# Kernel tuning notes

Measured on AMD Instinct MI355X. Metric: run time of the kernel, lower is better.

Reference implementation:

```python
import jax, jax.numpy as jnp
import numpy as np

KEY_DIM = 64
SCALE_PER_SEQ = 1.0 / np.sqrt(KEY_DIM).astype(np.float32)   # attn_scale_factor_per_seq default
SCALE_OVER_SEQS = 1.0 / np.sqrt(KEY_DIM).astype(np.float32) # attn_scale_factor_over_seqs default


def setup_inputs() -> dict:
    key = jax.random.key(0)
    ks = jax.random.split(key, 6)
    b, i, t, j, d = 8, 256, 64, 256, 256
    kd, vd = KEY_DIM, 64
    return {
        "input_seq": jax.random.normal(ks[0], (b, i, d), dtype=jnp.float32),
        "memory_x": jax.random.normal(ks[1], (b, t, j, d), dtype=jnp.float32),
        "memory_y": jax.random.normal(ks[2], (b, t, j, d), dtype=jnp.float32),
        "Wq": jax.random.normal(ks[3], (d, kd), dtype=jnp.float32) * (1.0 / np.sqrt(d)),
        "bq": jnp.zeros((kd,), dtype=jnp.float32),
        "Wk": jax.random.normal(ks[4], (d, kd), dtype=jnp.float32) * (1.0 / np.sqrt(d)),
        "bk": jnp.zeros((kd,), dtype=jnp.float32),
        "Wv": jax.random.normal(ks[5], (d, vd), dtype=jnp.float32) * (1.0 / np.sqrt(d)),
        "bv": jnp.zeros((vd,), dtype=jnp.float32),
    }


def reference(input_seq, memory_x, memory_y, Wq, bq, Wk, bk, Wv, bv):
    # Dense projections
    queries = input_seq @ Wq + bq            # [b, i, kd]
    keys = memory_x @ Wk + bk                # [b, t, j, kd]
    values = memory_y @ Wv + bv              # [b, t, j, vd]

    # Raw scores between every query and every token of every memory sequence
    attn_mat = jnp.einsum('bik,btjk->btij', queries, keys)  # [b, t, i, j]

    # Level 1: within-sequence attention (softmax over tokens j)
    per_seq_attn = jax.nn.softmax(SCALE_PER_SEQ * attn_mat, axis=-1)
    per_seq_retrieved = jnp.einsum('btij,btjk->btik', per_seq_attn, values)  # [b, t, i, vd]

    # Level 2: over-sequences attention (max over j, softmax over t)
    mem_seq_scores = jnp.max(attn_mat, axis=-1)                      # [b, t, i]
    mem_seq_attn = jax.nn.softmax(SCALE_OVER_SEQS * mem_seq_scores, axis=1)

    retrieved_mems = jnp.einsum('bti,btik->bik', mem_seq_attn, per_seq_retrieved)  # [b, i, vd]
    return retrieved_mems
```

## Files before the change

### kernel.cpp

```cpp
#include <hip/hip_runtime.h>
#include <hip/hip_bf16.h>

#define NB 8
#define NT 64
#define NI 256
#define NJ 256
#define ND 256
#define NKD 64
#define NVD 64
#define SCL 0.125f

typedef __attribute__((ext_vector_type(4))) float f32x4;
typedef __attribute__((ext_vector_type(8))) short bf16x8;
typedef __attribute__((ext_vector_type(4))) short bf16x4;
typedef __attribute__((ext_vector_type(4))) unsigned int uint32x4;

#define MFMA16(A, B, C) __builtin_amdgcn_mfma_f32_16x16x32_bf16((A), (B), (C), 0, 0, 0)

#define R2B 32768

__device__ __forceinline__ unsigned short f2bf(float x) {
  return __builtin_bit_cast(unsigned short, __float2bfloat16(x));
}
__device__ __forceinline__ float bf2f(unsigned short h) {
  return __builtin_bit_cast(float, (unsigned)h << 16);
}
__device__ __forceinline__ void split8(const float* __restrict__ x, bf16x8& hi, bf16x8& lo) {
  #pragma unroll
  for (int e = 0; e < 8; ++e) {
    unsigned short h = f2bf(x[e]);
    hi[e] = (short)h;
    lo[e] = (short)f2bf(x[e] - bf2f(h));
  }
}

__global__ __launch_bounds__(64) void k_prep_projq(
    const float* __restrict__ x, const float* __restrict__ Wq,
    const float* __restrict__ bq,
    const float* __restrict__ Wk, const float* __restrict__ Wv,
    unsigned short* __restrict__ Wkth,
    unsigned short* __restrict__ Wvth, unsigned short* __restrict__ Wvtl,
    unsigned short* __restrict__ Qh, unsigned short* __restrict__ Ql) {
  int lane = threadIdx.x;
  if (blockIdx.x < 256) {
    int t = blockIdx.x * 64 + lane;
    int d = t >> 6, kd = t & 63;
    Wkth[kd * 256 + d] = f2bf(Wk[t]);
    float v = Wv[t];
    unsigned short h = f2bf(v);
    Wvth[kd * 256 + d] = h;
    Wvtl[kd * 256 + d] = f2bf(v - bf2f(h));
    return;
  }
  int row = blockIdx.x - 256;
  __shared__ __align__(16) float xs[ND];
  const float* xr = x + (size_t)row * ND;
  #pragma unroll
  for (int cc = 0; cc < 4; ++cc) xs[lane + 64 * cc] = xr[lane + 64 * cc];
  __syncthreads();
  float acc = bq[lane];
  #pragma unroll 4
  for (int d = 0; d < ND; ++d) acc = fmaf(xs[d], Wq[d * NKD + lane], acc);
  unsigned short h = f2bf(acc);
  Qh[(size_t)row * NKD + lane] = h;
  Ql[(size_t)row * NKD + lane] = f2bf(acc - bf2f(h));
}

__device__ __forceinline__ void stage_plane(
    char* dstb, const unsigned short* __restrict__ Wt, int tid) {
  #pragma unroll
  for (int it = 0; it < 4; ++it) {
    int qq = tid + it * 512;
    int r = qq >> 5, pb = qq & 31;
    uint4 v = *(const uint4*)((const char*)Wt + (size_t)qq * 16);
    *(uint4*)(dstb + r * 512 + ((pb ^ (r & 7)) << 4)) = v;
  }
}

__global__ __launch_bounds__(512, 4) void k_fused(
    const float* __restrict__ Xm, const float* __restrict__ Ym,
    const unsigned short* __restrict__ Wkth,
    const unsigned short* __restrict__ Wvth, const unsigned short* __restrict__ Wvtl,
    const float* __restrict__ bk, const float* __restrict__ bv,
    const unsigned short* __restrict__ Qh, const unsigned short* __restrict__ Ql,
    unsigned short* __restrict__ R,
    float* __restrict__ Sc) {
  __shared__ __align__(16) char smemb[65536];
  int tid = threadIdx.x;
  int bt = blockIdx.x, b = bt >> 6;
  int w = tid >> 6, lane = tid & 63, c = lane & 15, g = lane >> 4;

  const float* yr0 = Ym + (size_t)bt * 65536 + (size_t)(w * 32 + c) * 256 + g * 8;
  const float* yr1 = yr0 + 16 * 256;
  const float* xr0 = Xm + (size_t)bt * 65536 + (size_t)(w * 32 + c) * 256 + g * 8;
  const float* xr1 = xr0 + 16 * 256;

  float4 pby[4][4];
  #pragma unroll
  for (int s = 0; s < 4; ++s) {
    pby[s][0] = *(const float4*)(yr0 + s * 32);
    pby[s][1] = *(const float4*)(yr0 + s * 32 + 4);
    pby[s][2] = *(const float4*)(yr1 + s * 32);
    pby[s][3] = *(const float4*)(yr1 + s * 32 + 4);
  }
  stage_plane(smemb, Wvth, tid);
  stage_plane(smemb + R2B, Wvtl, tid);
  __syncthreads();

  f32x4 vacc[2][4];
  #pragma unroll
  for (int mf = 0; mf < 2; ++mf)
    #pragma unroll
    for (int nf = 0; nf < 4; ++nf) vacc[mf][nf] = (f32x4)0.f;
  #pragma unroll
  for (int ks = 0; ks < 8; ++ks) {
    int s = ks & 3;
    float y0[8], y1[8];
    *(float4*)&y0[0] = pby[s][0]; *(float4*)&y0[4] = pby[s][1];
    *(float4*)&y1[0] = pby[s][2]; *(float4*)&y1[4] = pby[s][3];
    if (ks < 4) {
      pby[s][0] = *(const float4*)(yr0 + (ks + 4) * 32);
      pby[s][1] = *(const float4*)(yr0 + (ks + 4) * 32 + 4);
      pby[s][2] = *(const float4*)(yr1 + (ks + 4) * 32);
      pby[s][3] = *(const float4*)(yr1 + (ks + 4) * 32 + 4);
    }
    bf16x8 a0h, a0l, a1h, a1l;
    split8(y0, a0h, a0l);
    split8(y1, a1h, a1l);
    #pragma unroll
    for (int nf = 0; nf < 4; ++nf) {
      int r = nf * 16 + c;
      int ba = r * 512 + (((ks * 4 + g) ^ (r & 7)) << 4);
      bf16x8 bwh = *(const bf16x8*)(smemb + ba);
      bf16x8 bwl = *(const bf16x8*)(smemb + R2B + ba);
      vacc[0][nf] = MFMA16(a0h, bwh, vacc[0][nf]);
      vacc[0][nf] = MFMA16(a0l, bwh, vacc[0][nf]);
      vacc[0][nf] = MFMA16(a0h, bwl, vacc[0][nf]);
      vacc[1][nf] = MFMA16(a1h, bwh, vacc[1][nf]);
      vacc[1][nf] = MFMA16(a1l, bwh, vacc[1][nf]);
      vacc[1][nf] = MFMA16(a1h, bwl, vacc[1][nf]);
    }
  }
  __syncthreads();

  float4 pbx[4][4];
  #pragma unroll
  for (int s = 0; s < 4; ++s) {
    pbx[s][0] = *(const float4*)(xr0 + s * 32);
    pbx[s][1] = *(const float4*)(xr0 + s * 32 + 4);
    pbx[s][2] = *(const float4*)(xr1 + s * 32);
    pbx[s][3] = *(const float4*)(xr1 + s * 32 + 4);
  }
  #pragma unroll
  for (int nf = 0; nf < 4; ++nf) {
    int vd = nf * 16 + c;
    float bs = bv[vd];
    #pragma unroll
    for (int mf = 0; mf < 2; ++mf) {
      bf16x4 ph;
      #pragma unroll
      for (int r = 0; r < 4; ++r) ph[r] = (short)f2bf(vacc[mf][nf][r] + bs);
      int pb = w * 4 + mf * 2 + (g >> 1);
      int ba = R2B + vd * 512 + ((pb ^ (vd & 7)) << 4) + (g & 1) * 8;
      *(bf16x4*)(smemb + ba) = ph;
    }
  }
  stage_plane(smemb, Wkth, tid);
  __syncthreads();

  f32x4 kacc[4][2];
  #pragma unroll
  for (int mf = 0; mf < 4; ++mf) { kacc[mf][0] = (f32x4)0.f; kacc[mf][1] = (f32x4)0.f; }
  #pragma unroll
  for (int ks = 0; ks < 8; ++ks) {
    int s = ks & 3;
    float x0[8], x1[8];
    *(float4*)&x0[0] = pbx[s][0]; *(float4*)&x0[4] = pbx[s][1];
    *(float4*)&x1[0] = pbx[s][2]; *(float4*)&x1[4] = pbx[s][3];
    if (ks < 4) {
      pbx[s][0] = *(const float4*)(xr0 + (ks + 4) * 32);
      pbx[s][1] = *(const float4*)(xr0 + (ks + 4) * 32 + 4);
      pbx[s][2] = *(const float4*)(xr1 + (ks + 4) * 32);
      pbx[s][3] = *(const float4*)(xr1 + (ks + 4) * 32 + 4);
    }
    bf16x8 b0h, b0l, b1h, b1l;
    split8(x0, b0h, b0l);
    split8(x1, b1h, b1l);
    #pragma unroll
    for (int mf = 0; mf < 4; ++mf) {
      int r = mf * 16 + c;
      int ba = r * 512 + (((ks * 4 + g) ^ (r & 7)) << 4);
      bf16x8 awh = *(const bf16x8*)(smemb + ba);
      kacc[mf][0] = MFMA16(awh, b0h, kacc[mf][0]);
      kacc[mf][0] = MFMA16(awh, b0l, kacc[mf][0]);
      kacc[mf][1] = MFMA16(awh, b1h, kacc[mf][1]);
      kacc[mf][1] = MFMA16(awh, b1l, kacc[mf][1]);
    }
  }
  __syncthreads();

  bf16x8 qbh[2][2], qbl[2][2];
  #pragma unroll
  for (int ks = 0; ks < 2; ++ks)
    #pragma unroll
    for (int ic = 0; ic < 2; ++ic) {
      size_t qo = ((size_t)b * NI + w * 32 + ic * 16 + c) * NKD + ks * 32 + g * 8;
      qbh[ks][ic] = *(const bf16x8*)(Qh + qo);
      qbl[ks][ic] = *(const bf16x8*)(Ql + qo);
    }
  #pragma unroll
  for (int nf = 0; nf < 2; ++nf) {
    int j = w * 32 + nf * 16 + c;
    #pragma unroll
    for (int mf = 0; mf < 4; ++mf) {
      bf16x4 ph;
      #pragma unroll
      for (int r = 0; r < 4; ++r)
        ph[r] = (short)f2bf(kacc[mf][nf][r] + bk[mf * 16 + g * 4 + r]);
      int pb = mf * 2 + (g >> 1);
      int ba = j * 128 + ((pb ^ (j & 7)) << 4) + (g & 1) * 8;
      *(bf16x4*)(smemb + ba) = ph;
    }
  }
  __syncthreads();

  #pragma unroll
  for (int ic = 0; ic < 2; ++ic) {
    int i = w * 32 + ic * 16 + c;

    f32x4 sa[16];
    #pragma unroll
    for (int jf = 0; jf < 16; ++jf) sa[jf] = (f32x4)0.f;
    #pragma unroll
    for (int jf = 0; jf < 16; ++jf) {
      int j = jf * 16 + c;
      #pragma unroll
      for (int ks = 0; ks < 2; ++ks) {
        int ba = j * 128 + (((ks * 4 + g) ^ (j & 7)) << 4);
        bf16x8 kh = *(const bf16x8*)(smemb + ba);
        sa[jf] = MFMA16(kh, qbh[ks][ic], sa[jf]);
        sa[jf] = MFMA16(kh, qbl[ks][ic], sa[jf]);
      }
    }

    float mx = sa[0][0];
    #pragma unroll
    for (int jf = 0; jf < 16; ++jf)
      #pragma unroll
      for (int r = 0; r < 4; ++r) mx = fmaxf(mx, sa[jf][r]);
    mx = fmaxf(mx, __shfl_xor(mx, 16));
    mx = fmaxf(mx, __shfl_xor(mx, 32));
    if (g == 0) Sc[(size_t)bt * NI + i] = mx;
    float sum = 0.f;
    #pragma unroll
    for (int jf = 0; jf < 16; ++jf)
      #pragma unroll
      for (int r = 0; r < 4; ++r) {
        float p = __expf((sa[jf][r] - mx) * SCL);
        sa[jf][r] = p;
        sum += p;
      }
    sum += __shfl_xor(sum, 16);
    sum += __shfl_xor(sum, 32);
    float linv = 1.0f / sum;

    unsigned int plo[16], phi[16];
    #pragma unroll
    for (int jf = 0; jf < 16; ++jf) {
      plo[jf] = (unsigned int)f2bf(sa[jf][0]) | ((unsigned int)f2bf(sa[jf][1]) << 16);
      phi[jf] = (unsigned int)f2bf(sa[jf][2]) | ((unsigned int)f2bf(sa[jf][3]) << 16);
    }

    int srcA = c + 32 * (g & 1);
    int srcB = srcA + 16;
    bool hiH = (g >= 2);

    f32x4 racc[4];
    #pragma unroll
    for (int vf = 0; vf < 4; ++vf) racc[vf] = (f32x4)0.f;
    #pragma unroll
    for (int js = 0; js < 8; ++js) {
      int a0 = __shfl((int)plo[2 * js], srcA);
      int a1 = __shfl((int)phi[2 * js], srcA);
      int a2 = __shfl((int)plo[2 * js], srcB);
      int a3 = __shfl((int)phi[2 * js], srcB);
      int b0 = __shfl((int)plo[2 * js + 1], srcA);
      int b1 = __shfl((int)phi[2 * js + 1], srcA);
      int b2 = __shfl((int)plo[2 * js + 1], srcB);
      int b3 = __shfl((int)phi[2 * js + 1], srcB);
      uint32x4 pw;
      pw[0] = (unsigned int)(hiH ? b0 : a0);
      pw[1] = (unsigned int)(hiH ? b1 : a1);
      pw[2] = (unsigned int)(hiH ? b2 : a2);
      pw[3] = (unsigned int)(hiH ? b3 : a3);
      bf16x8 pf = __builtin_bit_cast(bf16x8, pw);
      #pragma unroll
      for (int vf = 0; vf < 4; ++vf) {
        int vd = vf * 16 + c;
        int vba = R2B + vd * 512 + (((js * 4 + g) ^ (vd & 7)) << 4);
        bf16x8 vh = *(const bf16x8*)(smemb + vba);
        racc[vf] = MFMA16(vh, pf, racc[vf]);
      }
    }

    #pragma unroll
    for (int vf = 0; vf < 4; ++vf) {
      bf16x4 rk;
      #pragma unroll
      for (int r = 0; r < 4; ++r) rk[r] = (short)f2bf(racc[vf][r] * linv);
      *(bf16x4*)(R + ((size_t)bt * NI + i) * NKD + vf * 16 + g * 4) = rk;
    }
  }
}

__global__ __launch_bounds__(256) void k_level2(
    const float* __restrict__ Sc,
    const unsigned short* __restrict__ R,
    float* __restrict__ out) {
  int w = threadIdx.x >> 6, lane = threadIdx.x & 63;
  int bi = blockIdx.x * 4 + w;
  int b = bi >> 8, i = bi & 255;
  float sc = Sc[((size_t)b * NT + lane) * NI + i];
  float mx = sc;
  #pragma unroll
  for (int off = 32; off; off >>= 1) mx = fmaxf(mx, __shfl_xor(mx, off));
  float e = __expf((sc - mx) * SCL);
  float sum = e;
  #pragma unroll
  for (int off = 32; off; off >>= 1) sum += __shfl_xor(sum, off);
  float wn = e / sum;
  float acc = 0.f;
  for (int t = 0; t < NT; ++t) {
    float wt = __shfl(wn, t);
    acc = fmaf(wt, bf2f(R[(((size_t)b * NT + t) * NI + i) * NKD + lane]), acc);
  }
  out[((size_t)b * NI + i) * NVD + lane] = acc;
}

extern "C" void kernel_launch(void* const* d_in, const int* in_sizes, int n_in,
                              void* d_out, int out_size, void* d_ws, size_t ws_size,
                              hipStream_t stream) {
  const float* x   = (const float*)d_in[0];
  const float* mxp = (const float*)d_in[1];
  const float* myp = (const float*)d_in[2];
  const float* Wq  = (const float*)d_in[3];
  const float* bq  = (const float*)d_in[4];
  const float* Wk  = (const float*)d_in[5];
  const float* bk  = (const float*)d_in[6];
  const float* Wv  = (const float*)d_in[7];
  const float* bv  = (const float*)d_in[8];
  float* out = (float*)d_out;

  char* p = (char*)d_ws;
  auto alloc = [&](size_t bytes) { char* r = p; p += (bytes + 255) & ~(size_t)255; return r; };
  unsigned short* Qh   = (unsigned short*)alloc(2048 * 64 * 2);
  unsigned short* Ql   = (unsigned short*)alloc(2048 * 64 * 2);
  unsigned short* Rw   = (unsigned short*)alloc((size_t)131072 * 64 * 2);
  float*          Scw  = (float*)alloc((size_t)131072 * 4);
  unsigned short* Wkth = (unsigned short*)alloc(64 * 256 * 2);
  unsigned short* Wvth = (unsigned short*)alloc(64 * 256 * 2);
  unsigned short* Wvtl = (unsigned short*)alloc(64 * 256 * 2);

  hipLaunchKernelGGL(k_prep_projq, dim3(256 + NB * NI), dim3(64), 0, stream,
                     x, Wq, bq, Wk, Wv, Wkth, Wvth, Wvtl, Qh, Ql);
  hipLaunchKernelGGL(k_fused, dim3(NB * NT), dim3(512), 0, stream,
                     mxp, myp, Wkth, Wvth, Wvtl, bk, bv, Qh, Ql, Rw, Scw);
  hipLaunchKernelGGL(k_level2, dim3(512), dim3(256), 0, stream, Scw, Rw, out);
}
```

Measured before the change: 96.59 us.

## Merge K and V projection loops and drop low-bf16 plane of Wv

The separate V-projection and K-projection phases are merged into one k-loop that interleaves X and Y loads, staging both Wk and Wv high planes in shared memory at once and removing an intermediate barrier. The Wv low-order bf16 correction term is dropped, so V uses two MFMAs per fragment instead of three, and the Wvtl buffer is removed. Prefetch depth is reduced to two k-steps per stream to fit registers. This cuts MFMA count, LDS staging and one sync, at the cost of slightly lower precision in the V projection and higher register pressure from holding both accumulator sets.

After: 96.68 us. About the same (+0.1%).

```diff
diff --git a/kernel.cpp b/kernel.cpp
--- a/kernel.cpp
+++ b/kernel.cpp
@@ -38,18 +38,14 @@
     const float* __restrict__ x, const float* __restrict__ Wq,
     const float* __restrict__ bq,
     const float* __restrict__ Wk, const float* __restrict__ Wv,
-    unsigned short* __restrict__ Wkth,
-    unsigned short* __restrict__ Wvth, unsigned short* __restrict__ Wvtl,
+    unsigned short* __restrict__ Wkth, unsigned short* __restrict__ Wvth,
     unsigned short* __restrict__ Qh, unsigned short* __restrict__ Ql) {
   int lane = threadIdx.x;
   if (blockIdx.x < 256) {
     int t = blockIdx.x * 64 + lane;
     int d = t >> 6, kd = t & 63;
     Wkth[kd * 256 + d] = f2bf(Wk[t]);
-    float v = Wv[t];
-    unsigned short h = f2bf(v);
-    Wvth[kd * 256 + d] = h;
-    Wvtl[kd * 256 + d] = f2bf(v - bf2f(h));
+    Wvth[kd * 256 + d] = f2bf(Wv[t]);
     return;
   }
   int row = blockIdx.x - 256;
@@ -79,8 +75,7 @@
 
 __global__ __launch_bounds__(512, 4) void k_fused(
     const float* __restrict__ Xm, const float* __restrict__ Ym,
-    const unsigned short* __restrict__ Wkth,
-    const unsigned short* __restrict__ Wvth, const unsigned short* __restrict__ Wvtl,
+    const unsigned short* __restrict__ Wkth, const unsigned short* __restrict__ Wvth,
     const float* __restrict__ bk, const float* __restrict__ bv,
     const unsigned short* __restrict__ Qh, const unsigned short* __restrict__ Ql,
     unsigned short* __restrict__ R,
@@ -90,115 +85,106 @@
   int bt = blockIdx.x, b = bt >> 6;
   int w = tid >> 6, lane = tid & 63, c = lane & 15, g = lane >> 4;
 
+  const float* xr0 = Xm + (size_t)bt * 65536 + (size_t)(w * 32 + c) * 256 + g * 8;
+  const float* xr1 = xr0 + 16 * 256;
   const float* yr0 = Ym + (size_t)bt * 65536 + (size_t)(w * 32 + c) * 256 + g * 8;
   const float* yr1 = yr0 + 16 * 256;
-  const float* xr0 = Xm + (size_t)bt * 65536 + (size_t)(w * 32 + c) * 256 + g * 8;
-  const float* xr1 = xr0 + 16 * 256;
-
-  float4 pby[4][4];
-  #pragma unroll
-  for (int s = 0; s < 4; ++s) {
-    pby[s][0] = *(const float4*)(yr0 + s * 32);
-    pby[s][1] = *(const float4*)(yr0 + s * 32 + 4);
-    pby[s][2] = *(const float4*)(yr1 + s * 32);
-    pby[s][3] = *(const float4*)(yr1 + s * 32 + 4);
-  }
-  stage_plane(smemb, Wvth, tid);
-  stage_plane(smemb + R2B, Wvtl, tid);
+
+  float4 xa0 = *(const float4*)(xr0),      xa1 = *(const float4*)(xr0 + 4);
+  float4 xa2 = *(const float4*)(xr1),      xa3 = *(const float4*)(xr1 + 4);
+  float4 xb0 = *(const float4*)(xr0 + 32), xb1 = *(const float4*)(xr0 + 36);
+  float4 xb2 = *(const float4*)(xr1 + 32), xb3 = *(const float4*)(xr1 + 36);
+  float4 ya0 = *(const float4*)(yr0),      ya1 = *(const float4*)(yr0 + 4);
+  float4 ya2 = *(const float4*)(yr1),      ya3 = *(const float4*)(yr1 + 4);
+  float4 yb0 = *(const float4*)(yr0 + 32), yb1 = *(const float4*)(yr0 + 36);
+  float4 yb2 = *(const float4*)(yr1 + 32), yb3 = *(const float4*)(yr1 + 36);
+
+  stage_plane(smemb, Wkth, tid);
+  stage_plane(smemb + R2B, Wvth, tid);
   __syncthreads();
 
+  f32x4 kacc[4][2];
   f32x4 vacc[2][4];
   #pragma unroll
+  for (int mf = 0; mf < 4; ++mf) { kacc[mf][0] = (f32x4)0.f; kacc[mf][1] = (f32x4)0.f; }
+  #pragma unroll
   for (int mf = 0; mf < 2; ++mf)
     #pragma unroll
     for (int nf = 0; nf < 4; ++nf) vacc[mf][nf] = (f32x4)0.f;
+
   #pragma unroll
   for (int ks = 0; ks < 8; ++ks) {
-    int s = ks & 3;
+    float x0[8], x1[8];
+    if (ks & 1) {
+      *(float4*)&x0[0] = xb0; *(float4*)&x0[4] = xb1;
+      *(float4*)&x1[0] = xb2; *(float4*)&x1[4] = xb3;
+      if (ks < 6) {
+        xb0 = *(const float4*)(xr0 + (ks + 2) * 32);
+        xb1 = *(const float4*)(xr0 + (ks + 2) * 32 + 4);
+        xb2 = *(const float4*)(xr1 + (ks + 2) * 32);
+        xb3 = *(const float4*)(xr1 + (ks + 2) * 32 + 4);
+      }
+    } else {
+      *(float4*)&x0[0] = xa0; *(float4*)&x0[4] = xa1;
+      *(float4*)&x1[0] = xa2; *(float4*)&x1[4] = xa3;
+      if (ks < 6) {
+        xa0 = *(const float4*)(xr0 + (ks + 2) * 32);
+        xa1 = *(const float4*)(xr0 + (ks + 2) * 32 + 4);
+        xa2 = *(const float4*)(xr1 + (ks + 2) * 32);
+        xa3 = *(const float4*)(xr1 + (ks + 2) * 32 + 4);
+      }
+    }
+    {
+      bf16x8 b0h, b0l, b1h, b1l;
+      split8(x0, b0h, b0l);
+      split8(x1, b1h, b1l);
+      #pragma unroll
+      for (int mf = 0; mf < 4; ++mf) {
+        int r = mf * 16 + c;
+        int ba = r * 512 + (((ks * 4 + g) ^ (r & 7)) << 4);
+        bf16x8 awh = *(const bf16x8*)(smemb + ba);
+        kacc[mf][0] = MFMA16(awh, b0h, kacc[mf][0]);
+        kacc[mf][0] = MFMA16(awh, b0l, kacc[mf][0]);
+        kacc[mf][1] = MFMA16(awh, b1h, kacc[mf][1]);
+        kacc[mf][1] = MFMA16(awh, b1l, kacc[mf][1]);
+      }
+    }
     float y0[8], y1[8];
-    *(float4*)&y0[0] = pby[s][0]; *(float4*)&y0[4] = pby[s][1];
-    *(float4*)&y1[0] = pby[s][2]; *(float4*)&y1[4] = pby[s][3];
-    if (ks < 4) {
-      pby[s][0] = *(const float4*)(yr0 + (ks + 4) * 32);
-      pby[s][1] = *(const float4*)(yr0 + (ks + 4) * 32 + 4);
-      pby[s][2] = *(const float4*)(yr1 + (ks + 4) * 32);
-      pby[s][3] = *(const float4*)(yr1 + (ks + 4) * 32 + 4);
-    }
-    bf16x8 a0h, a0l, a1h, a1l;
-    split8(y0, a0h, a0l);
-    split8(y1, a1h, a1l);
-    #pragma unroll
-    for (int nf = 0; nf < 4; ++nf) {
-      int r = nf * 16 + c;
-      int ba = r * 512 + (((ks * 4 + g) ^ (r & 7)) << 4);
-      bf16x8 bwh = *(const bf16x8*)(smemb + ba);
-      bf16x8 bwl = *(const bf16x8*)(smemb + R2B + ba);
-      vacc[0][nf] = MFMA16(a0h, bwh, vacc[0][nf]);
-      vacc[0][nf] = MFMA16(a0l, bwh, vacc[0][nf]);
-      vacc[0][nf] = MFMA16(a0h, bwl, vacc[0][nf]);
-      vacc[1][nf] = MFMA16(a1h, bwh, vacc[1][nf]);
-      vacc[1][nf] = MFMA16(a1l, bwh, vacc[1][nf]);
-      vacc[1][nf] = MFMA16(a1h, bwl, vacc[1][nf]);
-    }
-  }
-  __syncthreads();
-
-  float4 pbx[4][4];
-  #pragma unroll
-  for (int s = 0; s < 4; ++s) {
-    pbx[s][0] = *(const float4*)(xr0 + s * 32);
-    pbx[s][1] = *(const float4*)(xr0 + s * 32 + 4);
-    pbx[s][2] = *(const float4*)(xr1 + s * 32);
-    pbx[s][3] = *(const float4*)(xr1 + s * 32 + 4);
-  }
-  #pragma unroll
-  for (int nf = 0; nf < 4; ++nf) {
-    int vd = nf * 16 + c;
-    float bs = bv[vd];
-    #pragma unroll
-    for (int mf = 0; mf < 2; ++mf) {
-      bf16x4 ph;
-      #pragma unroll
-      for (int r = 0; r < 4; ++r) ph[r] = (short)f2bf(vacc[mf][nf][r] + bs);
-      int pb = w * 4 + mf * 2 + (g >> 1);
-      int ba = R2B + vd * 512 + ((pb ^ (vd & 7)) << 4) + (g & 1) * 8;
-      *(bf16x4*)(smemb + ba) = ph;
-    }
-  }
-  stage_plane(smemb, Wkth, tid);
-  __syncthreads();
-
-  f32x4 kacc[4][2];
-  #pragma unroll
-  for (int mf = 0; mf < 4; ++mf) { kacc[mf][0] = (f32x4)0.f; kacc[mf][1] = (f32x4)0.f; }
-  #pragma unroll
-  for (int ks = 0; ks < 8; ++ks) {
-    int s = ks & 3;
-    float x0[8], x1[8];
-    *(float4*)&x0[0] = pbx[s][0]; *(float4*)&x0[4] = pbx[s][1];
-    *(float4*)&x1[0] = pbx[s][2]; *(float4*)&x1[4] = pbx[s][3];
-    if (ks < 4) {
-      pbx[s][0] = *(const float4*)(xr0 + (ks + 4) * 32);
-      pbx[s][1] = *(const float4*)(xr0 + (ks + 4) * 32 + 4);
-      pbx[s][2] = *(const float4*)(xr1 + (ks + 4) * 32);
-      pbx[s][3] = *(const float4*)(xr1 + (ks + 4) * 32 + 4);
-    }
-    bf16x8 b0h, b0l, b1h, b1l;
-    split8(x0, b0h, b0l);
-    split8(x1, b1h, b1l);
-    #pragma unroll
-    for (int mf = 0; mf < 4; ++mf) {
-      int r = mf * 16 + c;
-      int ba = r * 512 + (((ks * 4 + g) ^ (r & 7)) << 4);
-      bf16x8 awh = *(const bf16x8*)(smemb + ba);
-      kacc[mf][0] = MFMA16(awh, b0h, kacc[mf][0]);
-      kacc[mf][0] = MFMA16(awh, b0l, kacc[mf][0]);
-      kacc[mf][1] = MFMA16(awh, b1h, kacc[mf][1]);
-      kacc[mf][1] = MFMA16(awh, b1l, kacc[mf][1]);
-    }
-  }
-  __syncthreads();
-
+    if (ks & 1) {
+      *(float4*)&y0[0] = yb0; *(float4*)&y0[4] = yb1;
+      *(float4*)&y1[0] = yb2; *(float4*)&y1[4] = yb3;
+      if (ks < 6) {
+        yb0 = *(const float4*)(yr0 + (ks + 2) * 32);
+        yb1 = *(const float4*)(yr0 + (ks + 2) * 32 + 4);
+        yb2 = *(const float4*)(yr1 + (ks + 2) * 32);
+        yb3 = *(const float4*)(yr1 + (ks + 2) * 32 + 4);
+      }
+    } else {
+      *(float4*)&y0[0] = ya0; *(float4*)&y0[4] = ya1;
+      *(float4*)&y1[0] = ya2; *(float4*)&y1[4] = ya3;
+      if (ks < 6) {
+        ya0 = *(const float4*)(yr0 + (ks + 2) * 32);
+        ya1 = *(const float4*)(yr0 + (ks + 2) * 32 + 4);
+        ya2 = *(const float4*)(yr1 + (ks + 2) * 32);
+        ya3 = *(const float4*)(yr1 + (ks + 2) * 32 + 4);
+      }
+    }
+    {
+      bf16x8 a0h, a0l, a1h, a1l;
+      split8(y0, a0h, a0l);
+      split8(y1, a1h, a1l);
+      #pragma unroll
+      for (int nf = 0; nf < 4; ++nf) {
+        int r = nf * 16 + c;
+        int ba = R2B + r * 512 + (((ks * 4 + g) ^ (r & 7)) << 4);
+        bf16x8 bwh = *(const bf16x8*)(smemb + ba);
+        vacc[0][nf] = MFMA16(a0h, bwh, vacc[0][nf]);
+        vacc[0][nf] = MFMA16(a0l, bwh, vacc[0][nf]);
+        vacc[1][nf] = MFMA16(a1h, bwh, vacc[1][nf]);
+        vacc[1][nf] = MFMA16(a1l, bwh, vacc[1][nf]);
+      }
+    }
+  }
   bf16x8 qbh[2][2], qbl[2][2];
   #pragma unroll
   for (int ks = 0; ks < 2; ++ks)
@@ -208,6 +194,8 @@
       qbh[ks][ic] = *(const bf16x8*)(Qh + qo);
       qbl[ks][ic] = *(const bf16x8*)(Ql + qo);
     }
+  __syncthreads();
+
   #pragma unroll
   for (int nf = 0; nf < 2; ++nf) {
     int j = w * 32 + nf * 16 + c;
@@ -219,6 +207,20 @@
         ph[r] = (short)f2bf(kacc[mf][nf][r] + bk[mf * 16 + g * 4 + r]);
       int pb = mf * 2 + (g >> 1);
       int ba = j * 128 + ((pb ^ (j & 7)) << 4) + (g & 1) * 8;
+      *(bf16x4*)(smemb + ba) = ph;
+    }
+  }
+  #pragma unroll
+  for (int nf = 0; nf < 4; ++nf) {
+    int vd = nf * 16 + c;
+    float bs = bv[vd];
+    #pragma unroll
+    for (int mf = 0; mf < 2; ++mf) {
+      bf16x4 ph;
+      #pragma unroll
+      for (int r = 0; r < 4; ++r) ph[r] = (short)f2bf(vacc[mf][nf][r] + bs);
+      int pb = w * 4 + mf * 2 + (g >> 1);
+      int ba = R2B + vd * 512 + ((pb ^ (vd & 7)) << 4) + (g & 1) * 8;
       *(bf16x4*)(smemb + ba) = ph;
     }
   }
@@ -359,11 +361,10 @@
   float*          Scw  = (float*)alloc((size_t)131072 * 4);
   unsigned short* Wkth = (unsigned short*)alloc(64 * 256 * 2);
   unsigned short* Wvth = (unsigned short*)alloc(64 * 256 * 2);
-  unsigned short* Wvtl = (unsigned short*)alloc(64 * 256 * 2);
 
   hipLaunchKernelGGL(k_prep_projq, dim3(256 + NB * NI), dim3(64), 0, stream,
-                     x, Wq, bq, Wk, Wv, Wkth, Wvth, Wvtl, Qh, Ql);
+                     x, Wq, bq, Wk, Wv, Wkth, Wvth, Qh, Ql);
   hipLaunchKernelGGL(k_fused, dim3(NB * NT), dim3(512), 0, stream,
-                     mxp, myp, Wkth, Wvth, Wvtl, bk, bv, Qh, Ql, Rw, Scw);
+                     mxp, myp, Wkth, Wvth, bk, bv, Qh, Ql, Rw, Scw);
   hipLaunchKernelGGL(k_level2, dim3(512), dim3(256), 0, stream, Scw, Rw, out);
 }
```
